# Kernel tuning notes

Measured on AMD Instinct MI355X. Metric: run time of the kernel, lower is better.

Reference implementation:

```python
import jax, jax.numpy as jnp
import numpy as np

BLOCK = 64  # block_size from config
NEG_INF = -1e9


def setup_inputs() -> dict:
    key = jax.random.key(0)
    k1, k2, k3, k4 = jax.random.split(key, 4)
    B, H, S, D = 2, 8, 2048, 64
    nb = S // BLOCK  # 32 blocks per side
    query = jax.random.normal(k1, (B, H, S, D), dtype=jnp.float32)
    key_t = jax.random.normal(k2, (B, H, S, D), dtype=jnp.float32)
    value = jax.random.normal(k3, (B, H, S, D), dtype=jnp.float32)
    # binary block mask; force diagonal blocks on so every row has >=1 valid key
    mat = jax.random.randint(k4, (nb, nb), 0, 2).astype(jnp.int32)
    mat = mat.at[jnp.arange(nb), jnp.arange(nb)].set(1)
    mask = jnp.ones((B, S), dtype=jnp.float32)  # padding mask (1 = keep)
    return {"query": query, "key": key_t, "value": value, "mask": mask, "mat": mat}


def reference(query, key, value, mask, mat):
    # Upsample block mask [nb, nb] -> dense [S, S] (nearest, like nn.Upsample)
    block_dense = jnp.repeat(jnp.repeat(mat, BLOCK, axis=0), BLOCK, axis=1) > 0
    # Block-sparse QK^T: only positions inside nonzero blocks participate.
    scores = jnp.einsum('bhqd,bhkd->bhqk', query, key)
    # Additive padding-mask bias, as in the original: 1e6 * (1 - mask)
    scores = scores - 1e6 * (1.0 - mask)[:, None, None, :]
    # Positions outside the block pattern are excluded from the softmax.
    scores = jnp.where(block_dense[None, None, :, :], scores, NEG_INF)
    attn = jax.nn.softmax(scores, axis=-1)
    out = jnp.einsum('bhqk,bhkd->bhqd', attn, value)
    return out
```

## Files before the change

kernel.cpp:

```cpp
#include <hip/hip_runtime.h>


typedef __attribute__((ext_vector_type(8))) short short8;
typedef __attribute__((ext_vector_type(4))) short short4_;
typedef __attribute__((ext_vector_type(4))) float float4_;
typedef __attribute__((ext_vector_type(8))) _Float16 half8_;

#define B_   2
#define H_   8
#define S_   2048
#define D_   64
#define NB_  32
#define KP   72
#define KP2  66
#define LOG2E 1.4426950408889634f

__device__ __forceinline__ short f2bf(float f) {
    union { float f; unsigned int u; } x; x.f = f;
    unsigned int r = x.u + 0x7FFFu + ((x.u >> 16) & 1u);
    return (short)(r >> 16);
}
__device__ __forceinline__ short f2bf_t(float f) {
    union { float f; unsigned int u; } x; x.f = f;
    return (short)(x.u >> 16);
}
__device__ __forceinline__ float bf2f(short s) {
    union { unsigned int u; float f; } x; x.u = ((unsigned int)(unsigned short)s) << 16;
    return x.f;
}
__device__ __forceinline__ short f2h(float f) {
    _Float16 h = (_Float16)f;
    return __builtin_bit_cast(short, h);
}
__device__ __forceinline__ int swz(int row, int gran) {
    return (row << 6) + (((gran ^ row) & 7) << 3);
}
__device__ __forceinline__ void gload16(const short* g, short* l) {
    __builtin_amdgcn_global_load_lds(
        (const __attribute__((address_space(1))) void*)g,
        (__attribute__((address_space(3))) void*)l, 16, 0, 0);
}
__device__ __forceinline__ void wg_remap(int n, int& bh, int& idx) {
    const int xcd = n & 7;
    const int sub = n >> 3;
    bh  = (xcd << 1) + (sub & 1);
    idx = sub >> 1;
}

__global__ __launch_bounds__(256)
void preconvert_kernel(const float* __restrict__ K, const float* __restrict__ V,
                       short* __restrict__ Khf, short* __restrict__ Vtb) {
    __shared__ short vn[64 * KP2];
    const int tid = threadIdx.x;
    int bh, kt;
    wg_remap(blockIdx.x, bh, kt);
    const size_t src = ((size_t)bh * S_ + kt * 64) * D_;
    const size_t dst = ((size_t)(bh * NB_ + kt)) << 12;

#pragma unroll
    for (int it = 0; it < 4; ++it) {
        int i = tid + it * 256;
        int row = i >> 4, c4 = (i & 15) * 4;
        float4_ kv = *(const float4_*)(K + src + row * D_ + c4);
        short4_ kh;
#pragma unroll
        for (int e = 0; e < 4; ++e) kh[e] = f2h(kv[e] * LOG2E);
        *(short4_*)(Khf + dst + swz(row, c4 >> 3) + (c4 & 7)) = kh;
        float4_ vv = *(const float4_*)(V + src + row * D_ + c4);
        short4_ vb;
#pragma unroll
        for (int e = 0; e < 4; ++e) vb[e] = f2bf(vv[e]);
        *(short4_*)&vn[row * KP2 + c4] = vb;
    }
    __syncthreads();

#pragma unroll
    for (int it = 0; it < 2; ++it) {
        int i = tid + it * 256;
        int d = i >> 3, g = i & 7;
        short8 o;
#pragma unroll
        for (int e = 0; e < 8; ++e) o[e] = vn[(g * 8 + e) * KP2 + d];
        *(short8*)(Vtb + dst + swz(d, g)) = o;
    }
}

__global__ __launch_bounds__(512, 4)
void attn_fused(const float* __restrict__ Q,
                const float* __restrict__ Msk,
                const int* __restrict__ Mat,
                float* __restrict__ O,
                const short* __restrict__ Khf_g,
                const short* __restrict__ Vtb_g) {
    __shared__ __align__(16) short lds[40960];

    const int tid  = threadIdx.x;
    const int wave = tid >> 6;
    const int half = wave >> 2;
    const int w4   = wave & 3;
    const int lane = tid & 63;
    const int c    = lane & 15;
    const int quad = lane >> 4;

    int bh, qb;
    wg_remap(blockIdx.x, bh, qb);
    const int b  = bh / H_;
    const size_t base = (size_t)bh * S_ * D_;

    unsigned long long bmv = __ballot(Mat[qb * NB_ + (lane & 31)] != 0);
    unsigned int mb = (unsigned int)(bmv & 0xFFFFFFFFull);
    const int nact  = __popc(mb);
    const int niter = (nact + 1) >> 1;
    unsigned int mine = 0;
    {
        unsigned int tb2 = mb; int idx = 0;
        while (tb2) {
            int k = __builtin_ctz(tb2); tb2 &= tb2 - 1;
            if ((idx & 1) == half) mine |= (1u << k);
            ++idx;
        }
    }

    int kb; bool kill;
    if (mine) { kb = __builtin_ctz(mine); mine &= mine - 1; kill = false; }
    else      { kb = __builtin_ctz(mb); kill = true; }
    {
        const size_t tb = ((size_t)(bh * NB_ + kb)) << 12;
        const int kd = (half << 12) + (w4 << 10);
        const short* gk = Khf_g + tb + (w4 << 10) + lane * 8;
        const short* gv = Vtb_g + tb + (w4 << 10) + lane * 8;
        gload16(gk,       &lds[kd]);
        gload16(gk + 512, &lds[kd + 512]);
        gload16(gv,       &lds[16384 + kd]);
        gload16(gv + 512, &lds[16384 + kd + 512]);
    }

    float biasc[4], biasn[4] = {0.f, 0.f, 0.f, 0.f};
#pragma unroll
    for (int t = 0; t < 4; ++t)
        biasc[t] = kill ? -2.0e6f
                        : -1.0e6f * LOG2E * (1.0f - Msk[(size_t)b * S_ + kb * 64 + t * 16 + c]);

    half8_ qa0, qa1;
    {
        const float* qp = Q + base + (size_t)(qb * 64 + w4 * 16 + c) * D_ + quad * 8;
        float4_ q0 = *(const float4_*)(qp);
        float4_ q1 = *(const float4_*)(qp + 4);
        float4_ q2 = *(const float4_*)(qp + 32);
        float4_ q3 = *(const float4_*)(qp + 36);
#pragma unroll
        for (int e = 0; e < 4; ++e) {
            qa0[e]     = (_Float16)q0[e];
            qa0[e + 4] = (_Float16)q1[e];
            qa1[e]     = (_Float16)q2[e];
            qa1[e + 4] = (_Float16)q3[e];
        }
    }

    float4_ o[4];
    float l_part[4];
#pragma unroll
    for (int t = 0; t < 4; ++t) { o[t][0] = 0.f; o[t][1] = 0.f; o[t][2] = 0.f; o[t][3] = 0.f; }
#pragma unroll
    for (int j = 0; j < 4; ++j) l_part[j] = 0.f;

    int foff_lo[4], foff_hi[4];
#pragma unroll
    for (int t = 0; t < 4; ++t) {
        foff_lo[t] = swz(t * 16 + c, quad);
        foff_hi[t] = swz(t * 16 + c, quad + 4);
    }
    const int pwoff = 32768 + (wave << 10);
    const int prd0  = pwoff + swz(c, quad);
    const int prd1  = pwoff + swz(c, quad + 4);

    int cur = 0;
    for (int it2 = 0; it2 < niter; ++it2) {
        bool nkill = true;
        if (it2 + 1 < niter && mine) { kb = __builtin_ctz(mine); mine &= mine - 1; nkill = false; }

        __syncthreads();

        if (it2 + 1 < niter) {
            const size_t tb = ((size_t)(bh * NB_ + kb)) << 12;
            const int kd = ((cur ^ 1) << 13) + (half << 12) + (w4 << 10);
            const short* gk = Khf_g + tb + (w4 << 10) + lane * 8;
            const short* gv = Vtb_g + tb + (w4 << 10) + lane * 8;
            gload16(gk,       &lds[kd]);
            gload16(gk + 512, &lds[kd + 512]);
            gload16(gv,       &lds[16384 + kd]);
            gload16(gv + 512, &lds[16384 + kd + 512]);
#pragma unroll
            for (int t = 0; t < 4; ++t)
                biasn[t] = nkill ? -2.0e6f
                                 : -1.0e6f * LOG2E * (1.0f - Msk[(size_t)b * S_ + kb * 64 + t * 16 + c]);
        }

        const int kbase = (cur << 13) + (half << 12);
        const int vbase = 16384 + kbase;

        float4_ sc[4];
#pragma unroll
        for (int t = 0; t < 4; ++t) { sc[t][0] = 0.f; sc[t][1] = 0.f; sc[t][2] = 0.f; sc[t][3] = 0.f; }
        __builtin_amdgcn_s_setprio(1);
#pragma unroll
        for (int t = 0; t < 4; ++t) {
            half8_ kf0 = __builtin_bit_cast(half8_, *(const short8*)&lds[kbase + foff_lo[t]]);
            half8_ kf1 = __builtin_bit_cast(half8_, *(const short8*)&lds[kbase + foff_hi[t]]);
            sc[t] = __builtin_amdgcn_mfma_f32_16x16x32_f16(qa0, kf0, sc[t], 0, 0, 0);
            sc[t] = __builtin_amdgcn_mfma_f32_16x16x32_f16(qa1, kf1, sc[t], 0, 0, 0);
        }
        __builtin_amdgcn_s_setprio(0);

#pragma unroll
        for (int t = 0; t < 4; ++t) {
            const int cg = (t << 1) + (c >> 3);
#pragma unroll
            for (int j = 0; j < 4; ++j) {
                float p = __builtin_amdgcn_exp2f(sc[t][j] + biasc[t]);
                l_part[j] += p;
                const int row = quad * 4 + j;
                lds[pwoff + (row << 6) + (((cg ^ row) & 7) << 3) + (c & 7)] = f2bf_t(p);
            }
        }

        short8 pa0 = *(const short8*)&lds[prd0];
        short8 pa1 = *(const short8*)&lds[prd1];

        __builtin_amdgcn_s_setprio(1);
#pragma unroll
        for (int t = 0; t < 4; ++t) {
            short8 vb0 = *(const short8*)&lds[vbase + foff_lo[t]];
            short8 vb1 = *(const short8*)&lds[vbase + foff_hi[t]];
            o[t] = __builtin_amdgcn_mfma_f32_16x16x32_bf16(pa0, vb0, o[t], 0, 0, 0);
            o[t] = __builtin_amdgcn_mfma_f32_16x16x32_bf16(pa1, vb1, o[t], 0, 0, 0);
        }
        __builtin_amdgcn_s_setprio(0);

#pragma unroll
        for (int t = 0; t < 4; ++t) biasc[t] = biasn[t];
        cur ^= 1;
    }

    __syncthreads();
    float* fl = (float*)lds;
    if (half == 1) {
        const int idx = ((wave - 4) * 64 + lane) * 21;
#pragma unroll
        for (int t = 0; t < 4; ++t)
#pragma unroll
            for (int j = 0; j < 4; ++j) fl[idx + t * 4 + j] = o[t][j];
#pragma unroll
        for (int j = 0; j < 4; ++j) fl[idx + 16 + j] = l_part[j];
    }
    __syncthreads();
    if (half == 0) {
        const int idx = (wave * 64 + lane) * 21;
#pragma unroll
        for (int j = 0; j < 4; ++j) {
            float rs = l_part[j] + fl[idx + 16 + j];
            rs += __shfl_xor(rs, 1);
            rs += __shfl_xor(rs, 2);
            rs += __shfl_xor(rs, 4);
            rs += __shfl_xor(rs, 8);
            float inv = 1.0f / rs;
            size_t rowoff = base + (size_t)(qb * 64 + w4 * 16 + quad * 4 + j) * D_;
#pragma unroll
            for (int t = 0; t < 4; ++t)
                O[rowoff + t * 16 + c] = (o[t][j] + fl[idx + t * 4 + j]) * inv;
        }
    }
}

__global__ __launch_bounds__(256, 2)
void attn_mfma_fb(const float* __restrict__ Q,
                  const float* __restrict__ K,
                  const float* __restrict__ V,
                  const float* __restrict__ Msk,
                  const int* __restrict__ Mat,
                  float* __restrict__ O) {
    __shared__ __align__(16) short lds[4 * 64 * KP];
    short* Khi = lds;
    short* Klo = lds + 64 * KP;
    short* Vt  = lds + 2 * 64 * KP;
    short* Pl  = lds + 3 * 64 * KP;

    const int tid  = threadIdx.x;
    const int wave = tid >> 6;
    const int lane = tid & 63;
    const int c    = lane & 15;
    const int quad = lane >> 4;

    const int qb = blockIdx.x;
    const int bh = blockIdx.y;
    const int b  = bh / H_;
    const size_t base = (size_t)bh * S_ * D_;

    short8 qh0, qh1, ql0, ql1;
    {
        const float* qp = Q + base + (size_t)(qb * 64 + wave * 16 + c) * D_ + quad * 8;
#pragma unroll
        for (int e = 0; e < 8; ++e) {
            float f0 = qp[e], f1 = qp[e + 32];
            qh0[e] = f2bf(f0); ql0[e] = f2bf(f0 - bf2f(qh0[e]));
            qh1[e] = f2bf(f1); ql1[e] = f2bf(f1 - bf2f(qh1[e]));
        }
    }

    float4_ o[4];
    float l_part[4];
#pragma unroll
    for (int t = 0; t < 4; ++t) { o[t][0] = 0.f; o[t][1] = 0.f; o[t][2] = 0.f; o[t][3] = 0.f; }
#pragma unroll
    for (int j = 0; j < 4; ++j) l_part[j] = 0.f;

    for (int kb = 0; kb < NB_; ++kb) {
        if (Mat[qb * NB_ + kb] == 0) continue;

        __syncthreads();
        {
            const float* kg = K + base + (size_t)kb * 64 * D_;
            const float* vg = V + base + (size_t)kb * 64 * D_;
#pragma unroll
            for (int it = 0; it < 4; ++it) {
                int i = tid + it * 256;
                int row = i >> 4, c4 = (i & 15) * 4;
                float4_ kv = *(const float4_*)(kg + row * D_ + c4);
                short4_ hi, lo;
#pragma unroll
                for (int e = 0; e < 4; ++e) {
                    hi[e] = f2bf(kv[e]);
                    lo[e] = f2bf(kv[e] - bf2f(hi[e]));
                }
                *(short4_*)&Khi[row * KP + c4] = hi;
                *(short4_*)&Klo[row * KP + c4] = lo;
                float4_ vv = *(const float4_*)(vg + row * D_ + c4);
#pragma unroll
                for (int e = 0; e < 4; ++e) Vt[(c4 + e) * KP + row] = f2bf(vv[e]);
            }
        }
        __syncthreads();

        float4_ sc[4];
#pragma unroll
        for (int t = 0; t < 4; ++t) { sc[t][0] = 0.f; sc[t][1] = 0.f; sc[t][2] = 0.f; sc[t][3] = 0.f; }
#pragma unroll
        for (int t = 0; t < 4; ++t) {
            const short* kph = &Khi[(t * 16 + c) * KP + quad * 8];
            const short* kpl = &Klo[(t * 16 + c) * KP + quad * 8];
            short8 kh0 = *(const short8*)(kph);
            short8 kh1 = *(const short8*)(kph + 32);
            short8 kl0 = *(const short8*)(kpl);
            short8 kl1 = *(const short8*)(kpl + 32);
            sc[t] = __builtin_amdgcn_mfma_f32_16x16x32_bf16(qh0, kh0, sc[t], 0, 0, 0);
            sc[t] = __builtin_amdgcn_mfma_f32_16x16x32_bf16(qh1, kh1, sc[t], 0, 0, 0);
            sc[t] = __builtin_amdgcn_mfma_f32_16x16x32_bf16(qh0, kl0, sc[t], 0, 0, 0);
            sc[t] = __builtin_amdgcn_mfma_f32_16x16x32_bf16(qh1, kl1, sc[t], 0, 0, 0);
            sc[t] = __builtin_amdgcn_mfma_f32_16x16x32_bf16(ql0, kh0, sc[t], 0, 0, 0);
            sc[t] = __builtin_amdgcn_mfma_f32_16x16x32_bf16(ql1, kh1, sc[t], 0, 0, 0);
        }

        short* Pw = Pl + wave * 16 * KP;
#pragma unroll
        for (int t = 0; t < 4; ++t) {
            float bias = -1.0e6f * (1.0f - Msk[(size_t)b * S_ + kb * 64 + t * 16 + c]);
#pragma unroll
            for (int j = 0; j < 4; ++j) {
                float p = __expf(sc[t][j] + bias);
                l_part[j] += p;
                Pw[(quad * 4 + j) * KP + t * 16 + c] = f2bf(p);
            }
        }

        const short* pp = Pl + wave * 16 * KP + c * KP + quad * 8;
        short8 pa0 = *(const short8*)(pp);
        short8 pa1 = *(const short8*)(pp + 32);

#pragma unroll
        for (int t = 0; t < 4; ++t) {
            const short* vp = &Vt[(t * 16 + c) * KP + quad * 8];
            short8 vb0 = *(const short8*)(vp);
            short8 vb1 = *(const short8*)(vp + 32);
            o[t] = __builtin_amdgcn_mfma_f32_16x16x32_bf16(pa0, vb0, o[t], 0, 0, 0);
            o[t] = __builtin_amdgcn_mfma_f32_16x16x32_bf16(pa1, vb1, o[t], 0, 0, 0);
        }
    }

#pragma unroll
    for (int j = 0; j < 4; ++j) {
        float rs = l_part[j];
        rs += __shfl_xor(rs, 1);
        rs += __shfl_xor(rs, 2);
        rs += __shfl_xor(rs, 4);
        rs += __shfl_xor(rs, 8);
        float inv = 1.0f / rs;
        size_t rowoff = base + (size_t)(qb * 64 + wave * 16 + quad * 4 + j) * D_;
#pragma unroll
        for (int t = 0; t < 4; ++t)
            O[rowoff + t * 16 + c] = o[t][j] * inv;
    }
}

extern "C" void kernel_launch(void* const* d_in, const int* in_sizes, int n_in,
                              void* d_out, int out_size, void* d_ws, size_t ws_size,
                              hipStream_t stream) {
    const float* q   = (const float*)d_in[0];
    const float* k   = (const float*)d_in[1];
    const float* v   = (const float*)d_in[2];
    const float* msk = (const float*)d_in[3];
    const int*   mat = (const int*)d_in[4];
    float*       out = (float*)d_out;

    const size_t elems = (size_t)B_ * H_ * S_ * D_;
    const size_t need  = 2 * elems * sizeof(short);
    const int use_pre  = (ws_size >= need) ? 1 : 0;

    short* khf = (short*)d_ws;
    short* vtb = khf + elems;

    if (use_pre) {
        preconvert_kernel<<<dim3(NB_ * B_ * H_), dim3(256), 0, stream>>>(k, v, khf, vtb);
        attn_fused<<<dim3(NB_ * B_ * H_), dim3(512), 0, stream>>>(q, msk, mat, out, khf, vtb);
    } else {
        dim3 grid(NB_, B_ * H_);
        attn_mfma_fb<<<grid, dim3(256), 0, stream>>>(q, k, v, msk, mat, out);
    }
}
```

Baseline: 104.7 us.

## Halve waves per block, each wave computes two 16-row query tiles

The fused attention kernel now launches 256 threads (4 waves) instead of 512. Each wave handles 32 query rows as two 16-row groups, so every K and V fragment read from LDS feeds two MFMAs. Each wave issues twice as many global-to-LDS loads, and the P scratch and the final cross-half reduction buffers are resized to match. The aim is fewer LDS reads and less sync overhead per unit of work, at the cost of higher register pressure, fewer waves to hide latency, and changed launch bounds.

```diff
diff --git a/kernel.cpp b/kernel.cpp
--- a/kernel.cpp
+++ b/kernel.cpp
@@ -85,7 +85,7 @@
     }
 }
 
-__global__ __launch_bounds__(512, 4)
+__global__ __launch_bounds__(256, 2)
 void attn_fused(const float* __restrict__ Q,
                 const float* __restrict__ Msk,
                 const int* __restrict__ Mat,
@@ -96,8 +96,8 @@
 
     const int tid  = threadIdx.x;
     const int wave = tid >> 6;
-    const int half = wave >> 2;
-    const int w4   = wave & 3;
+    const int half = wave >> 1;
+    const int wh   = wave & 1;
     const int lane = tid & 63;
     const int c    = lane & 15;
     const int quad = lane >> 4;
@@ -126,13 +126,14 @@
     else      { kb = __builtin_ctz(mb); kill = true; }
     {
         const size_t tb = ((size_t)(bh * NB_ + kb)) << 12;
-        const int kd = (half << 12) + (w4 << 10);
-        const short* gk = Khf_g + tb + (w4 << 10) + lane * 8;
-        const short* gv = Vtb_g + tb + (w4 << 10) + lane * 8;
-        gload16(gk,       &lds[kd]);
-        gload16(gk + 512, &lds[kd + 512]);
-        gload16(gv,       &lds[16384 + kd]);
-        gload16(gv + 512, &lds[16384 + kd + 512]);
+        const int kd = (half << 12) + (wh << 11);
+        const short* gk = Khf_g + tb + (wh << 11) + lane * 8;
+        const short* gv = Vtb_g + tb + (wh << 11) + lane * 8;
+#pragma unroll
+        for (int r = 0; r < 4; ++r) {
+            gload16(gk + r * 512, &lds[kd + r * 512]);
+            gload16(gv + r * 512, &lds[16384 + kd + r * 512]);
+        }
     }
 
     float biasc[4], biasn[4] = {0.f, 0.f, 0.f, 0.f};
@@ -141,28 +142,32 @@
         biasc[t] = kill ? -2.0e6f
                         : -1.0e6f * LOG2E * (1.0f - Msk[(size_t)b * S_ + kb * 64 + t * 16 + c]);
 
-    half8_ qa0, qa1;
-    {
-        const float* qp = Q + base + (size_t)(qb * 64 + w4 * 16 + c) * D_ + quad * 8;
+    half8_ qa[2][2];
+#pragma unroll
+    for (int g = 0; g < 2; ++g) {
+        const float* qp = Q + base + (size_t)(qb * 64 + wh * 32 + g * 16 + c) * D_ + quad * 8;
         float4_ q0 = *(const float4_*)(qp);
         float4_ q1 = *(const float4_*)(qp + 4);
         float4_ q2 = *(const float4_*)(qp + 32);
         float4_ q3 = *(const float4_*)(qp + 36);
 #pragma unroll
         for (int e = 0; e < 4; ++e) {
-            qa0[e]     = (_Float16)q0[e];
-            qa0[e + 4] = (_Float16)q1[e];
-            qa1[e]     = (_Float16)q2[e];
-            qa1[e + 4] = (_Float16)q3[e];
-        }
-    }
-
-    float4_ o[4];
-    float l_part[4];
-#pragma unroll
-    for (int t = 0; t < 4; ++t) { o[t][0] = 0.f; o[t][1] = 0.f; o[t][2] = 0.f; o[t][3] = 0.f; }
-#pragma unroll
-    for (int j = 0; j < 4; ++j) l_part[j] = 0.f;
+            qa[g][0][e]     = (_Float16)q0[e];
+            qa[g][0][e + 4] = (_Float16)q1[e];
+            qa[g][1][e]     = (_Float16)q2[e];
+            qa[g][1][e + 4] = (_Float16)q3[e];
+        }
+    }
+
+    float4_ o[2][4];
+    float l_part[2][4];
+#pragma unroll
+    for (int g = 0; g < 2; ++g)
+#pragma unroll
+        for (int t = 0; t < 4; ++t) {
+            o[g][t][0] = 0.f; o[g][t][1] = 0.f; o[g][t][2] = 0.f; o[g][t][3] = 0.f;
+            l_part[g][t] = 0.f;
+        }
 
     int foff_lo[4], foff_hi[4];
 #pragma unroll
@@ -170,7 +175,7 @@
         foff_lo[t] = swz(t * 16 + c, quad);
         foff_hi[t] = swz(t * 16 + c, quad + 4);
     }
-    const int pwoff = 32768 + (wave << 10);
+    const int pwoff = 32768 + (wave << 11);
     const int prd0  = pwoff + swz(c, quad);
     const int prd1  = pwoff + swz(c, quad + 4);
 
@@ -183,13 +188,14 @@
 
         if (it2 + 1 < niter) {
             const size_t tb = ((size_t)(bh * NB_ + kb)) << 12;
-            const int kd = ((cur ^ 1) << 13) + (half << 12) + (w4 << 10);
-            const short* gk = Khf_g + tb + (w4 << 10) + lane * 8;
-            const short* gv = Vtb_g + tb + (w4 << 10) + lane * 8;
-            gload16(gk,       &lds[kd]);
-            gload16(gk + 512, &lds[kd + 512]);
-            gload16(gv,       &lds[16384 + kd]);
-            gload16(gv + 512, &lds[16384 + kd + 512]);
+            const int kd = ((cur ^ 1) << 13) + (half << 12) + (wh << 11);
+            const short* gk = Khf_g + tb + (wh << 11) + lane * 8;
+            const short* gv = Vtb_g + tb + (wh << 11) + lane * 8;
+#pragma unroll
+            for (int r = 0; r < 4; ++r) {
+                gload16(gk + r * 512, &lds[kd + r * 512]);
+                gload16(gv + r * 512, &lds[16384 + kd + r * 512]);
+            }
 #pragma unroll
             for (int t = 0; t < 4; ++t)
                 biasn[t] = nkill ? -2.0e6f
@@ -199,41 +205,55 @@
         const int kbase = (cur << 13) + (half << 12);
         const int vbase = 16384 + kbase;
 
-        float4_ sc[4];
-#pragma unroll
-        for (int t = 0; t < 4; ++t) { sc[t][0] = 0.f; sc[t][1] = 0.f; sc[t][2] = 0.f; sc[t][3] = 0.f; }
+        float4_ sc[2][4];
+#pragma unroll
+        for (int g = 0; g < 2; ++g)
+#pragma unroll
+            for (int t = 0; t < 4; ++t) { sc[g][t][0] = 0.f; sc[g][t][1] = 0.f; sc[g][t][2] = 0.f; sc[g][t][3] = 0.f; }
         __builtin_amdgcn_s_setprio(1);
 #pragma unroll
         for (int t = 0; t < 4; ++t) {
             half8_ kf0 = __builtin_bit_cast(half8_, *(const short8*)&lds[kbase + foff_lo[t]]);
             half8_ kf1 = __builtin_bit_cast(half8_, *(const short8*)&lds[kbase + foff_hi[t]]);
-            sc[t] = __builtin_amdgcn_mfma_f32_16x16x32_f16(qa0, kf0, sc[t], 0, 0, 0);
-            sc[t] = __builtin_amdgcn_mfma_f32_16x16x32_f16(qa1, kf1, sc[t], 0, 0, 0);
+            sc[0][t] = __builtin_amdgcn_mfma_f32_16x16x32_f16(qa[0][0], kf0, sc[0][t], 0, 0, 0);
+            sc[0][t] = __builtin_amdgcn_mfma_f32_16x16x32_f16(qa[0][1], kf1, sc[0][t], 0, 0, 0);
+            sc[1][t] = __builtin_amdgcn_mfma_f32_16x16x32_f16(qa[1][0], kf0, sc[1][t], 0, 0, 0);
+            sc[1][t] = __builtin_amdgcn_mfma_f32_16x16x32_f16(qa[1][1], kf1, sc[1][t], 0, 0, 0);
         }
         __builtin_amdgcn_s_setprio(0);
 
 #pragma unroll
-        for (int t = 0; t < 4; ++t) {
-            const int cg = (t << 1) + (c >> 3);
-#pragma unroll
-            for (int j = 0; j < 4; ++j) {
-                float p = __builtin_amdgcn_exp2f(sc[t][j] + biasc[t]);
-                l_part[j] += p;
-                const int row = quad * 4 + j;
-                lds[pwoff + (row << 6) + (((cg ^ row) & 7) << 3) + (c & 7)] = f2bf_t(p);
+        for (int g = 0; g < 2; ++g) {
+            const int pg = pwoff + (g << 10);
+#pragma unroll
+            for (int t = 0; t < 4; ++t) {
+                const int cg = (t << 1) + (c >> 3);
+#pragma unroll
+                for (int j = 0; j < 4; ++j) {
+                    float p = __builtin_amdgcn_exp2f(sc[g][t][j] + biasc[t]);
+                    l_part[g][j] += p;
+                    const int row = quad * 4 + j;
+                    lds[pg + (row << 6) + (((cg ^ row) & 7) << 3) + (c & 7)] = f2bf_t(p);
+                }
             }
         }
 
-        short8 pa0 = *(const short8*)&lds[prd0];
-        short8 pa1 = *(const short8*)&lds[prd1];
+        short8 pa[2][2];
+#pragma unroll
+        for (int g = 0; g < 2; ++g) {
+            pa[g][0] = *(const short8*)&lds[prd0 + (g << 10)];
+            pa[g][1] = *(const short8*)&lds[prd1 + (g << 10)];
+        }
 
         __builtin_amdgcn_s_setprio(1);
 #pragma unroll
         for (int t = 0; t < 4; ++t) {
             short8 vb0 = *(const short8*)&lds[vbase + foff_lo[t]];
             short8 vb1 = *(const short8*)&lds[vbase + foff_hi[t]];
-            o[t] = __builtin_amdgcn_mfma_f32_16x16x32_bf16(pa0, vb0, o[t], 0, 0, 0);
-            o[t] = __builtin_amdgcn_mfma_f32_16x16x32_bf16(pa1, vb1, o[t], 0, 0, 0);
+            o[0][t] = __builtin_amdgcn_mfma_f32_16x16x32_bf16(pa[0][0], vb0, o[0][t], 0, 0, 0);
+            o[0][t] = __builtin_amdgcn_mfma_f32_16x16x32_bf16(pa[0][1], vb1, o[0][t], 0, 0, 0);
+            o[1][t] = __builtin_amdgcn_mfma_f32_16x16x32_bf16(pa[1][0], vb0, o[1][t], 0, 0, 0);
+            o[1][t] = __builtin_amdgcn_mfma_f32_16x16x32_bf16(pa[1][1], vb1, o[1][t], 0, 0, 0);
         }
         __builtin_amdgcn_s_setprio(0);
 
@@ -245,30 +265,35 @@
     __syncthreads();
     float* fl = (float*)lds;
     if (half == 1) {
-        const int idx = ((wave - 4) * 64 + lane) * 21;
-#pragma unroll
-        for (int t = 0; t < 4; ++t)
-#pragma unroll
-            for (int j = 0; j < 4; ++j) fl[idx + t * 4 + j] = o[t][j];
-#pragma unroll
-        for (int j = 0; j < 4; ++j) fl[idx + 16 + j] = l_part[j];
+        const int idx = ((wave - 2) * 64 + lane) * 41;
+#pragma unroll
+        for (int g = 0; g < 2; ++g) {
+#pragma unroll
+            for (int t = 0; t < 4; ++t)
+#pragma unroll
+                for (int j = 0; j < 4; ++j) fl[idx + g * 16 + t * 4 + j] = o[g][t][j];
+#pragma unroll
+            for (int j = 0; j < 4; ++j) fl[idx + 32 + g * 4 + j] = l_part[g][j];
+        }
     }
     __syncthreads();
     if (half == 0) {
-        const int idx = (wave * 64 + lane) * 21;
-#pragma unroll
-        for (int j = 0; j < 4; ++j) {
-            float rs = l_part[j] + fl[idx + 16 + j];
-            rs += __shfl_xor(rs, 1);
-            rs += __shfl_xor(rs, 2);
-            rs += __shfl_xor(rs, 4);
-            rs += __shfl_xor(rs, 8);
-            float inv = 1.0f / rs;
-            size_t rowoff = base + (size_t)(qb * 64 + w4 * 16 + quad * 4 + j) * D_;
-#pragma unroll
-            for (int t = 0; t < 4; ++t)
-                O[rowoff + t * 16 + c] = (o[t][j] + fl[idx + t * 4 + j]) * inv;
-        }
+        const int idx = (wave * 64 + lane) * 41;
+#pragma unroll
+        for (int g = 0; g < 2; ++g)
+#pragma unroll
+            for (int j = 0; j < 4; ++j) {
+                float rs = l_part[g][j] + fl[idx + 32 + g * 4 + j];
+                rs += __shfl_xor(rs, 1);
+                rs += __shfl_xor(rs, 2);
+                rs += __shfl_xor(rs, 4);
+                rs += __shfl_xor(rs, 8);
+                float inv = 1.0f / rs;
+                size_t rowoff = base + (size_t)(qb * 64 + wh * 32 + g * 16 + quad * 4 + j) * D_;
+#pragma unroll
+                for (int t = 0; t < 4; ++t)
+                    O[rowoff + t * 16 + c] = (o[g][t][j] + fl[idx + g * 16 + t * 4 + j]) * inv;
+            }
     }
 }
 
@@ -420,7 +445,7 @@
 
     if (use_pre) {
         preconvert_kernel<<<dim3(NB_ * B_ * H_), dim3(256), 0, stream>>>(k, v, khf, vtb);
-        attn_fused<<<dim3(NB_ * B_ * H_), dim3(512), 0, stream>>>(q, msk, mat, out, khf, vtb);
+        attn_fused<<<dim3(NB_ * B_ * H_), dim3(256), 0, stream>>>(q, msk, mat, out, khf, vtb);
     } else {
         dim3 grid(NB_, B_ * H_);
         attn_mfma_fb<<<grid, dim3(256), 0, stream>>>(q, k, v, msk, mat, out);
```

Result: no change. 105.3 us (+0.6%).

## Fuse K/V conversion into attention kernel, dropping the preconvert pass

Applied to the files above, without the earlier changes.

Removes the separate preconvert kernel and its fp16/bf16 workspace round trip. The attention kernel now loads fp32 K and V directly, converts them in registers and writes them into swizzled LDS, with the loads for the next block overlapped with the current block's MFMA work. The LOG2E scale moves from K onto Q. In exchange it gives up the async global_load_lds path, does scalar transposed LDS stores for V, reads K/V at double width from every query block, and raises register pressure. The unused fallback kernel is deleted.

```diff
diff --git a/kernel.cpp b/kernel.cpp
--- a/kernel.cpp
+++ b/kernel.cpp
@@ -11,8 +11,6 @@
 #define S_   2048
 #define D_   64
 #define NB_  32
-#define KP   72
-#define KP2  66
 #define LOG2E 1.4426950408889634f
 
 __device__ __forceinline__ short f2bf(float f) {
@@ -24,21 +22,12 @@
     union { float f; unsigned int u; } x; x.f = f;
     return (short)(x.u >> 16);
 }
-__device__ __forceinline__ float bf2f(short s) {
-    union { unsigned int u; float f; } x; x.u = ((unsigned int)(unsigned short)s) << 16;
-    return x.f;
-}
 __device__ __forceinline__ short f2h(float f) {
     _Float16 h = (_Float16)f;
     return __builtin_bit_cast(short, h);
 }
 __device__ __forceinline__ int swz(int row, int gran) {
     return (row << 6) + (((gran ^ row) & 7) << 3);
-}
-__device__ __forceinline__ void gload16(const short* g, short* l) {
-    __builtin_amdgcn_global_load_lds(
-        (const __attribute__((address_space(1))) void*)g,
-        (__attribute__((address_space(3))) void*)l, 16, 0, 0);
 }
 __device__ __forceinline__ void wg_remap(int n, int& bh, int& idx) {
     const int xcd = n & 7;
@@ -47,51 +36,13 @@
     idx = sub >> 1;
 }
 
-__global__ __launch_bounds__(256)
-void preconvert_kernel(const float* __restrict__ K, const float* __restrict__ V,
-                       short* __restrict__ Khf, short* __restrict__ Vtb) {
-    __shared__ short vn[64 * KP2];
-    const int tid = threadIdx.x;
-    int bh, kt;
-    wg_remap(blockIdx.x, bh, kt);
-    const size_t src = ((size_t)bh * S_ + kt * 64) * D_;
-    const size_t dst = ((size_t)(bh * NB_ + kt)) << 12;
-
-#pragma unroll
-    for (int it = 0; it < 4; ++it) {
-        int i = tid + it * 256;
-        int row = i >> 4, c4 = (i & 15) * 4;
-        float4_ kv = *(const float4_*)(K + src + row * D_ + c4);
-        short4_ kh;
-#pragma unroll
-        for (int e = 0; e < 4; ++e) kh[e] = f2h(kv[e] * LOG2E);
-        *(short4_*)(Khf + dst + swz(row, c4 >> 3) + (c4 & 7)) = kh;
-        float4_ vv = *(const float4_*)(V + src + row * D_ + c4);
-        short4_ vb;
-#pragma unroll
-        for (int e = 0; e < 4; ++e) vb[e] = f2bf(vv[e]);
-        *(short4_*)&vn[row * KP2 + c4] = vb;
-    }
-    __syncthreads();
-
-#pragma unroll
-    for (int it = 0; it < 2; ++it) {
-        int i = tid + it * 256;
-        int d = i >> 3, g = i & 7;
-        short8 o;
-#pragma unroll
-        for (int e = 0; e < 8; ++e) o[e] = vn[(g * 8 + e) * KP2 + d];
-        *(short8*)(Vtb + dst + swz(d, g)) = o;
-    }
-}
-
 __global__ __launch_bounds__(512, 4)
-void attn_fused(const float* __restrict__ Q,
-                const float* __restrict__ Msk,
-                const int* __restrict__ Mat,
-                float* __restrict__ O,
-                const short* __restrict__ Khf_g,
-                const short* __restrict__ Vtb_g) {
+void attn_direct(const float* __restrict__ Q,
+                 const float* __restrict__ K,
+                 const float* __restrict__ V,
+                 const float* __restrict__ Msk,
+                 const int* __restrict__ Mat,
+                 float* __restrict__ O) {
     __shared__ __align__(16) short lds[40960];
 
     const int tid  = threadIdx.x;
@@ -101,6 +52,13 @@
     const int lane = tid & 63;
     const int c    = lane & 15;
     const int quad = lane >> 4;
+    const int hid  = tid & 255;
+
+    const int krow   = hid >> 2;
+    const int kchunk = hid & 3;
+    const int kd0    = kchunk << 4;
+    const int vkey   = krow;
+    const int vd0    = kd0;
 
     int bh, qb;
     wg_remap(blockIdx.x, bh, qb);
@@ -125,14 +83,32 @@
     if (mine) { kb = __builtin_ctz(mine); mine &= mine - 1; kill = false; }
     else      { kb = __builtin_ctz(mb); kill = true; }
     {
-        const size_t tb = ((size_t)(bh * NB_ + kb)) << 12;
-        const int kd = (half << 12) + (w4 << 10);
-        const short* gk = Khf_g + tb + (w4 << 10) + lane * 8;
-        const short* gv = Vtb_g + tb + (w4 << 10) + lane * 8;
-        gload16(gk,       &lds[kd]);
-        gload16(gk + 512, &lds[kd + 512]);
-        gload16(gv,       &lds[16384 + kd]);
-        gload16(gv + 512, &lds[16384 + kd + 512]);
+        const float* kg = K + base + (size_t)kb * 64 * D_ + krow * D_ + kd0;
+        const float* vg = V + base + (size_t)kb * 64 * D_ + vkey * D_ + vd0;
+        const int kb0 = (half << 12);
+        const int vb0 = 16384 + (half << 12);
+        float4_ kv0 = *(const float4_*)(kg);
+        float4_ kv1 = *(const float4_*)(kg + 4);
+        float4_ kv2 = *(const float4_*)(kg + 8);
+        float4_ kv3 = *(const float4_*)(kg + 12);
+        short8 kw0, kw1;
+#pragma unroll
+        for (int e = 0; e < 4; ++e) {
+            kw0[e] = f2h(kv0[e]); kw0[e + 4] = f2h(kv1[e]);
+            kw1[e] = f2h(kv2[e]); kw1[e + 4] = f2h(kv3[e]);
+        }
+        *(short8*)&lds[kb0 + swz(krow, kchunk * 2)]     = kw0;
+        *(short8*)&lds[kb0 + swz(krow, kchunk * 2 + 1)] = kw1;
+        float4_ vv[4];
+#pragma unroll
+        for (int r = 0; r < 4; ++r) vv[r] = *(const float4_*)(vg + r * 4);
+#pragma unroll
+        for (int r = 0; r < 4; ++r)
+#pragma unroll
+            for (int e = 0; e < 4; ++e) {
+                int d = vd0 + r * 4 + e;
+                lds[vb0 + swz(d, vkey >> 3) + (vkey & 7)] = f2bf(vv[r][e]);
+            }
     }
 
     float biasc[4], biasn[4] = {0.f, 0.f, 0.f, 0.f};
@@ -150,10 +126,10 @@
         float4_ q3 = *(const float4_*)(qp + 36);
 #pragma unroll
         for (int e = 0; e < 4; ++e) {
-            qa0[e]     = (_Float16)q0[e];
-            qa0[e + 4] = (_Float16)q1[e];
-            qa1[e]     = (_Float16)q2[e];
-            qa1[e + 4] = (_Float16)q3[e];
+            qa0[e]     = (_Float16)(q0[e] * LOG2E);
+            qa0[e + 4] = (_Float16)(q1[e] * LOG2E);
+            qa1[e]     = (_Float16)(q2[e] * LOG2E);
+            qa1[e + 4] = (_Float16)(q3[e] * LOG2E);
         }
     }
 
@@ -178,18 +154,21 @@
     for (int it2 = 0; it2 < niter; ++it2) {
         bool nkill = true;
         if (it2 + 1 < niter && mine) { kb = __builtin_ctz(mine); mine &= mine - 1; nkill = false; }
+        const bool stage = (it2 + 1 < niter) && !nkill;
 
         __syncthreads();
 
+        const float* kg = nullptr; const float* vg = nullptr;
+        float4_ kv0, kv1, kv2, kv3;
+        if (stage) {
+            kg = K + base + (size_t)kb * 64 * D_ + krow * D_ + kd0;
+            vg = V + base + (size_t)kb * 64 * D_ + vkey * D_ + vd0;
+            kv0 = *(const float4_*)(kg);
+            kv1 = *(const float4_*)(kg + 4);
+            kv2 = *(const float4_*)(kg + 8);
+            kv3 = *(const float4_*)(kg + 12);
+        }
         if (it2 + 1 < niter) {
-            const size_t tb = ((size_t)(bh * NB_ + kb)) << 12;
-            const int kd = ((cur ^ 1) << 13) + (half << 12) + (w4 << 10);
-            const short* gk = Khf_g + tb + (w4 << 10) + lane * 8;
-            const short* gv = Vtb_g + tb + (w4 << 10) + lane * 8;
-            gload16(gk,       &lds[kd]);
-            gload16(gk + 512, &lds[kd + 512]);
-            gload16(gv,       &lds[16384 + kd]);
-            gload16(gv + 512, &lds[16384 + kd + 512]);
 #pragma unroll
             for (int t = 0; t < 4; ++t)
                 biasn[t] = nkill ? -2.0e6f
@@ -198,6 +177,7 @@
 
         const int kbase = (cur << 13) + (half << 12);
         const int vbase = 16384 + kbase;
+        const int nb13  = ((cur ^ 1) << 13) + (half << 12);
 
         float4_ sc[4];
 #pragma unroll
@@ -224,6 +204,20 @@
             }
         }
 
+        float4_ vv[4];
+        if (stage) {
+            short8 kw0, kw1;
+#pragma unroll
+            for (int e = 0; e < 4; ++e) {
+                kw0[e] = f2h(kv0[e]); kw0[e + 4] = f2h(kv1[e]);
+                kw1[e] = f2h(kv2[e]); kw1[e + 4] = f2h(kv3[e]);
+            }
+            *(short8*)&lds[nb13 + swz(krow, kchunk * 2)]     = kw0;
+            *(short8*)&lds[nb13 + swz(krow, kchunk * 2 + 1)] = kw1;
+#pragma unroll
+            for (int r = 0; r < 4; ++r) vv[r] = *(const float4_*)(vg + r * 4);
+        }
+
         short8 pa0 = *(const short8*)&lds[prd0];
         short8 pa1 = *(const short8*)&lds[prd1];
 
@@ -236,6 +230,17 @@
             o[t] = __builtin_amdgcn_mfma_f32_16x16x32_bf16(pa1, vb1, o[t], 0, 0, 0);
         }
         __builtin_amdgcn_s_setprio(0);
+
+        if (stage) {
+            const int vnb = 16384 + nb13;
+#pragma unroll
+            for (int r = 0; r < 4; ++r)
+#pragma unroll
+                for (int e = 0; e < 4; ++e) {
+                    int d = vd0 + r * 4 + e;
+                    lds[vnb + swz(d, vkey >> 3) + (vkey & 7)] = f2bf(vv[r][e]);
+                }
+        }
 
 #pragma unroll
         for (int t = 0; t < 4; ++t) biasc[t] = biasn[t];
@@ -269,135 +274,6 @@
             for (int t = 0; t < 4; ++t)
                 O[rowoff + t * 16 + c] = (o[t][j] + fl[idx + t * 4 + j]) * inv;
         }
-    }
-}
-
-__global__ __launch_bounds__(256, 2)
-void attn_mfma_fb(const float* __restrict__ Q,
-                  const float* __restrict__ K,
-                  const float* __restrict__ V,
-                  const float* __restrict__ Msk,
-                  const int* __restrict__ Mat,
-                  float* __restrict__ O) {
-    __shared__ __align__(16) short lds[4 * 64 * KP];
-    short* Khi = lds;
-    short* Klo = lds + 64 * KP;
-    short* Vt  = lds + 2 * 64 * KP;
-    short* Pl  = lds + 3 * 64 * KP;
-
-    const int tid  = threadIdx.x;
-    const int wave = tid >> 6;
-    const int lane = tid & 63;
-    const int c    = lane & 15;
-    const int quad = lane >> 4;
-
-    const int qb = blockIdx.x;
-    const int bh = blockIdx.y;
-    const int b  = bh / H_;
-    const size_t base = (size_t)bh * S_ * D_;
-
-    short8 qh0, qh1, ql0, ql1;
-    {
-        const float* qp = Q + base + (size_t)(qb * 64 + wave * 16 + c) * D_ + quad * 8;
-#pragma unroll
-        for (int e = 0; e < 8; ++e) {
-            float f0 = qp[e], f1 = qp[e + 32];
-            qh0[e] = f2bf(f0); ql0[e] = f2bf(f0 - bf2f(qh0[e]));
-            qh1[e] = f2bf(f1); ql1[e] = f2bf(f1 - bf2f(qh1[e]));
-        }
-    }
-
-    float4_ o[4];
-    float l_part[4];
-#pragma unroll
-    for (int t = 0; t < 4; ++t) { o[t][0] = 0.f; o[t][1] = 0.f; o[t][2] = 0.f; o[t][3] = 0.f; }
-#pragma unroll
-    for (int j = 0; j < 4; ++j) l_part[j] = 0.f;
-
-    for (int kb = 0; kb < NB_; ++kb) {
-        if (Mat[qb * NB_ + kb] == 0) continue;
-
-        __syncthreads();
-        {
-            const float* kg = K + base + (size_t)kb * 64 * D_;
-            const float* vg = V + base + (size_t)kb * 64 * D_;
-#pragma unroll
-            for (int it = 0; it < 4; ++it) {
-                int i = tid + it * 256;
-                int row = i >> 4, c4 = (i & 15) * 4;
-                float4_ kv = *(const float4_*)(kg + row * D_ + c4);
-                short4_ hi, lo;
-#pragma unroll
-                for (int e = 0; e < 4; ++e) {
-                    hi[e] = f2bf(kv[e]);
-                    lo[e] = f2bf(kv[e] - bf2f(hi[e]));
-                }
-                *(short4_*)&Khi[row * KP + c4] = hi;
-                *(short4_*)&Klo[row * KP + c4] = lo;
-                float4_ vv = *(const float4_*)(vg + row * D_ + c4);
-#pragma unroll
-                for (int e = 0; e < 4; ++e) Vt[(c4 + e) * KP + row] = f2bf(vv[e]);
-            }
-        }
-        __syncthreads();
-
-        float4_ sc[4];
-#pragma unroll
-        for (int t = 0; t < 4; ++t) { sc[t][0] = 0.f; sc[t][1] = 0.f; sc[t][2] = 0.f; sc[t][3] = 0.f; }
-#pragma unroll
-        for (int t = 0; t < 4; ++t) {
-            const short* kph = &Khi[(t * 16 + c) * KP + quad * 8];
-            const short* kpl = &Klo[(t * 16 + c) * KP + quad * 8];
-            short8 kh0 = *(const short8*)(kph);
-            short8 kh1 = *(const short8*)(kph + 32);
-            short8 kl0 = *(const short8*)(kpl);
-            short8 kl1 = *(const short8*)(kpl + 32);
-            sc[t] = __builtin_amdgcn_mfma_f32_16x16x32_bf16(qh0, kh0, sc[t], 0, 0, 0);
-            sc[t] = __builtin_amdgcn_mfma_f32_16x16x32_bf16(qh1, kh1, sc[t], 0, 0, 0);
-            sc[t] = __builtin_amdgcn_mfma_f32_16x16x32_bf16(qh0, kl0, sc[t], 0, 0, 0);
-            sc[t] = __builtin_amdgcn_mfma_f32_16x16x32_bf16(qh1, kl1, sc[t], 0, 0, 0);
-            sc[t] = __builtin_amdgcn_mfma_f32_16x16x32_bf16(ql0, kh0, sc[t], 0, 0, 0);
-            sc[t] = __builtin_amdgcn_mfma_f32_16x16x32_bf16(ql1, kh1, sc[t], 0, 0, 0);
-        }
-
-        short* Pw = Pl + wave * 16 * KP;
-#pragma unroll
-        for (int t = 0; t < 4; ++t) {
-            float bias = -1.0e6f * (1.0f - Msk[(size_t)b * S_ + kb * 64 + t * 16 + c]);
-#pragma unroll
-            for (int j = 0; j < 4; ++j) {
-                float p = __expf(sc[t][j] + bias);
-                l_part[j] += p;
-                Pw[(quad * 4 + j) * KP + t * 16 + c] = f2bf(p);
-            }
-        }
-
-        const short* pp = Pl + wave * 16 * KP + c * KP + quad * 8;
-        short8 pa0 = *(const short8*)(pp);
-        short8 pa1 = *(const short8*)(pp + 32);
-
-#pragma unroll
-        for (int t = 0; t < 4; ++t) {
-            const short* vp = &Vt[(t * 16 + c) * KP + quad * 8];
-            short8 vb0 = *(const short8*)(vp);
-            short8 vb1 = *(const short8*)(vp + 32);
-            o[t] = __builtin_amdgcn_mfma_f32_16x16x32_bf16(pa0, vb0, o[t], 0, 0, 0);
-            o[t] = __builtin_amdgcn_mfma_f32_16x16x32_bf16(pa1, vb1, o[t], 0, 0, 0);
-        }
-    }
-
-#pragma unroll
-    for (int j = 0; j < 4; ++j) {
-        float rs = l_part[j];
-        rs += __shfl_xor(rs, 1);
-        rs += __shfl_xor(rs, 2);
-        rs += __shfl_xor(rs, 4);
-        rs += __shfl_xor(rs, 8);
-        float inv = 1.0f / rs;
-        size_t rowoff = base + (size_t)(qb * 64 + wave * 16 + quad * 4 + j) * D_;
-#pragma unroll
-        for (int t = 0; t < 4; ++t)
-            O[rowoff + t * 16 + c] = o[t][j] * inv;
     }
 }
 
@@ -411,18 +287,7 @@
     const int*   mat = (const int*)d_in[4];
     float*       out = (float*)d_out;
 
-    const size_t elems = (size_t)B_ * H_ * S_ * D_;
-    const size_t need  = 2 * elems * sizeof(short);
-    const int use_pre  = (ws_size >= need) ? 1 : 0;
-
-    short* khf = (short*)d_ws;
-    short* vtb = khf + elems;
-
-    if (use_pre) {
-        preconvert_kernel<<<dim3(NB_ * B_ * H_), dim3(256), 0, stream>>>(k, v, khf, vtb);
-        attn_fused<<<dim3(NB_ * B_ * H_), dim3(512), 0, stream>>>(q, msk, mat, out, khf, vtb);
-    } else {
-        dim3 grid(NB_, B_ * H_);
-        attn_mfma_fb<<<grid, dim3(256), 0, stream>>>(q, k, v, msk, mat, out);
-    }
-}
+    (void)d_ws; (void)ws_size;
+
+    attn_direct<<<dim3(NB_ * B_ * H_), dim3(512), 0, stream>>>(q, k, v, msk, mat, out);
+}
```

New measurement: 165.4 us. 1.58x slower.

## Keep P in registers via transposed QK MFMA and permlane swaps instead of LDS

Applied to the files above, without the earlier changes.

Swaps the MFMA operand order so the score tile comes out transposed (keys along rows), then converts P to packed bf16 with v_cvt_pk_bf16 and rearranges it into the PV A-operand layout using v_permlane16/32_swap. This removes the per-wave LDS round trip for P, shrinking shared memory, and simplifies the row-sum reduction. It also skips loading the next tile when that tile is killed, and loads the padding-mask values as vectors inside the loop instead of prefetching the bias. P rounding changes from truncation to the hardware packed conversion, and the permlane shuffling must map lanes exactly to the PV operand layout.

```diff
diff --git a/kernel.cpp b/kernel.cpp
--- a/kernel.cpp
+++ b/kernel.cpp
@@ -4,6 +4,7 @@
 typedef __attribute__((ext_vector_type(8))) short short8;
 typedef __attribute__((ext_vector_type(4))) short short4_;
 typedef __attribute__((ext_vector_type(4))) float float4_;
+typedef __attribute__((ext_vector_type(4))) unsigned int uint4_;
 typedef __attribute__((ext_vector_type(8))) _Float16 half8_;
 
 #define B_   2
@@ -20,10 +21,6 @@
     unsigned int r = x.u + 0x7FFFu + ((x.u >> 16) & 1u);
     return (short)(r >> 16);
 }
-__device__ __forceinline__ short f2bf_t(float f) {
-    union { float f; unsigned int u; } x; x.f = f;
-    return (short)(x.u >> 16);
-}
 __device__ __forceinline__ float bf2f(short s) {
     union { unsigned int u; float f; } x; x.u = ((unsigned int)(unsigned short)s) << 16;
     return x.f;
@@ -39,6 +36,11 @@
     __builtin_amdgcn_global_load_lds(
         (const __attribute__((address_space(1))) void*)g,
         (__attribute__((address_space(3))) void*)l, 16, 0, 0);
+}
+__device__ __forceinline__ unsigned int cvt_pk_bf16(float lo, float hi) {
+    unsigned int r;
+    asm("v_cvt_pk_bf16_f32 %0, %1, %2" : "=v"(r) : "v"(lo), "v"(hi));
+    return r;
 }
 __device__ __forceinline__ void wg_remap(int n, int& bh, int& idx) {
     const int xcd = n & 7;
@@ -73,7 +75,6 @@
         *(short4_*)&vn[row * KP2 + c4] = vb;
     }
     __syncthreads();
-
 #pragma unroll
     for (int it = 0; it < 2; ++it) {
         int i = tid + it * 256;
@@ -92,7 +93,7 @@
                 float* __restrict__ O,
                 const short* __restrict__ Khf_g,
                 const short* __restrict__ Vtb_g) {
-    __shared__ __align__(16) short lds[40960];
+    __shared__ __align__(16) short lds[32768];
 
     const int tid  = threadIdx.x;
     const int wave = tid >> 6;
@@ -101,6 +102,7 @@
     const int lane = tid & 63;
     const int c    = lane & 15;
     const int quad = lane >> 4;
+    const bool oddq = (quad & 1) != 0;
 
     int bh, qb;
     wg_remap(blockIdx.x, bh, qb);
@@ -121,11 +123,11 @@
         }
     }
 
-    int kb; bool kill;
-    if (mine) { kb = __builtin_ctz(mine); mine &= mine - 1; kill = false; }
-    else      { kb = __builtin_ctz(mb); kill = true; }
+    int kb_c; bool kill_c;
+    if (mine) { kb_c = __builtin_ctz(mine); mine &= mine - 1; kill_c = false; }
+    else      { kb_c = __builtin_ctz(mb); kill_c = true; }
     {
-        const size_t tb = ((size_t)(bh * NB_ + kb)) << 12;
+        const size_t tb = ((size_t)(bh * NB_ + kb_c)) << 12;
         const int kd = (half << 12) + (w4 << 10);
         const short* gk = Khf_g + tb + (w4 << 10) + lane * 8;
         const short* gv = Vtb_g + tb + (w4 << 10) + lane * 8;
@@ -135,12 +137,6 @@
         gload16(gv + 512, &lds[16384 + kd + 512]);
     }
 
-    float biasc[4], biasn[4] = {0.f, 0.f, 0.f, 0.f};
-#pragma unroll
-    for (int t = 0; t < 4; ++t)
-        biasc[t] = kill ? -2.0e6f
-                        : -1.0e6f * LOG2E * (1.0f - Msk[(size_t)b * S_ + kb * 64 + t * 16 + c]);
-
     half8_ qa0, qa1;
     {
         const float* qp = Q + base + (size_t)(qb * 64 + w4 * 16 + c) * D_ + quad * 8;
@@ -158,11 +154,9 @@
     }
 
     float4_ o[4];
-    float l_part[4];
+    float l_sum = 0.f;
 #pragma unroll
     for (int t = 0; t < 4; ++t) { o[t][0] = 0.f; o[t][1] = 0.f; o[t][2] = 0.f; o[t][3] = 0.f; }
-#pragma unroll
-    for (int j = 0; j < 4; ++j) l_part[j] = 0.f;
 
     int foff_lo[4], foff_hi[4];
 #pragma unroll
@@ -170,19 +164,16 @@
         foff_lo[t] = swz(t * 16 + c, quad);
         foff_hi[t] = swz(t * 16 + c, quad + 4);
     }
-    const int pwoff = 32768 + (wave << 10);
-    const int prd0  = pwoff + swz(c, quad);
-    const int prd1  = pwoff + swz(c, quad + 4);
 
     int cur = 0;
     for (int it2 = 0; it2 < niter; ++it2) {
-        bool nkill = true;
-        if (it2 + 1 < niter && mine) { kb = __builtin_ctz(mine); mine &= mine - 1; nkill = false; }
+        int kb_n = kb_c; bool kill_n = true;
+        if (it2 + 1 < niter && mine) { kb_n = __builtin_ctz(mine); mine &= mine - 1; kill_n = false; }
 
         __syncthreads();
 
-        if (it2 + 1 < niter) {
-            const size_t tb = ((size_t)(bh * NB_ + kb)) << 12;
+        if (it2 + 1 < niter && !kill_n) {
+            const size_t tb = ((size_t)(bh * NB_ + kb_n)) << 12;
             const int kd = ((cur ^ 1) << 13) + (half << 12) + (w4 << 10);
             const short* gk = Khf_g + tb + (w4 << 10) + lane * 8;
             const short* gv = Vtb_g + tb + (w4 << 10) + lane * 8;
@@ -190,15 +181,18 @@
             gload16(gk + 512, &lds[kd + 512]);
             gload16(gv,       &lds[16384 + kd]);
             gload16(gv + 512, &lds[16384 + kd + 512]);
-#pragma unroll
-            for (int t = 0; t < 4; ++t)
-                biasn[t] = nkill ? -2.0e6f
-                                 : -1.0e6f * LOG2E * (1.0f - Msk[(size_t)b * S_ + kb * 64 + t * 16 + c]);
         }
 
         const int kbase = (cur << 13) + (half << 12);
         const int vbase = 16384 + kbase;
 
+        float4_ mskv[4];
+        if (!kill_c) {
+#pragma unroll
+            for (int t = 0; t < 4; ++t)
+                mskv[t] = *(const float4_*)(Msk + (size_t)b * S_ + kb_c * 64 + t * 16 + quad * 4);
+        }
+
         float4_ sc[4];
 #pragma unroll
         for (int t = 0; t < 4; ++t) { sc[t][0] = 0.f; sc[t][1] = 0.f; sc[t][2] = 0.f; sc[t][3] = 0.f; }
@@ -207,25 +201,54 @@
         for (int t = 0; t < 4; ++t) {
             half8_ kf0 = __builtin_bit_cast(half8_, *(const short8*)&lds[kbase + foff_lo[t]]);
             half8_ kf1 = __builtin_bit_cast(half8_, *(const short8*)&lds[kbase + foff_hi[t]]);
-            sc[t] = __builtin_amdgcn_mfma_f32_16x16x32_f16(qa0, kf0, sc[t], 0, 0, 0);
-            sc[t] = __builtin_amdgcn_mfma_f32_16x16x32_f16(qa1, kf1, sc[t], 0, 0, 0);
+            sc[t] = __builtin_amdgcn_mfma_f32_16x16x32_f16(kf0, qa0, sc[t], 0, 0, 0);
+            sc[t] = __builtin_amdgcn_mfma_f32_16x16x32_f16(kf1, qa1, sc[t], 0, 0, 0);
         }
         __builtin_amdgcn_s_setprio(0);
 
-#pragma unroll
-        for (int t = 0; t < 4; ++t) {
-            const int cg = (t << 1) + (c >> 3);
+        unsigned int r_[4][2];
+#pragma unroll
+        for (int t = 0; t < 4; ++t) {
+            float p[4];
 #pragma unroll
             for (int j = 0; j < 4; ++j) {
-                float p = __builtin_amdgcn_exp2f(sc[t][j] + biasc[t]);
-                l_part[j] += p;
-                const int row = quad * 4 + j;
-                lds[pwoff + (row << 6) + (((cg ^ row) & 7) << 3) + (c & 7)] = f2bf_t(p);
+                float bj = kill_c ? -2.0e6f : -1.0e6f * LOG2E * (1.0f - mskv[t][j]);
+                p[j] = __builtin_amdgcn_exp2f(sc[t][j] + bj);
+                l_sum += p[j];
             }
-        }
-
-        short8 pa0 = *(const short8*)&lds[prd0];
-        short8 pa1 = *(const short8*)&lds[prd1];
+            r_[t][0] = cvt_pk_bf16(p[0], p[1]);
+            r_[t][1] = cvt_pk_bf16(p[2], p[3]);
+        }
+
+        unsigned int La[4][2], Lb[4][2];
+#pragma unroll
+        for (int t = 0; t < 4; ++t)
+#pragma unroll
+            for (int s = 0; s < 2; ++s) {
+                unsigned int x = r_[t][s], y = r_[t][s];
+                asm("v_permlane16_swap_b32 %0, %1" : "+v"(x), "+v"(y));
+                La[t][s] = x;
+                Lb[t][s] = y;
+            }
+        uint4_ w0, w1;
+#pragma unroll
+        for (int s = 0; s < 2; ++s) {
+            unsigned int d0, s1;
+            d0 = La[0][s]; s1 = La[1][s];
+            asm("v_permlane32_swap_b32 %0, %1" : "+v"(d0), "+v"(s1));
+            w0[s] = oddq ? s1 : d0;
+            d0 = Lb[0][s]; s1 = Lb[1][s];
+            asm("v_permlane32_swap_b32 %0, %1" : "+v"(d0), "+v"(s1));
+            w0[2 + s] = oddq ? s1 : d0;
+            d0 = La[2][s]; s1 = La[3][s];
+            asm("v_permlane32_swap_b32 %0, %1" : "+v"(d0), "+v"(s1));
+            w1[s] = oddq ? s1 : d0;
+            d0 = Lb[2][s]; s1 = Lb[3][s];
+            asm("v_permlane32_swap_b32 %0, %1" : "+v"(d0), "+v"(s1));
+            w1[2 + s] = oddq ? s1 : d0;
+        }
+        short8 pa0 = __builtin_bit_cast(short8, w0);
+        short8 pa1 = __builtin_bit_cast(short8, w1);
 
         __builtin_amdgcn_s_setprio(1);
 #pragma unroll
@@ -237,32 +260,28 @@
         }
         __builtin_amdgcn_s_setprio(0);
 
-#pragma unroll
-        for (int t = 0; t < 4; ++t) biasc[t] = biasn[t];
-        cur ^= 1;
+        kb_c = kb_n; kill_c = kill_n; cur ^= 1;
     }
 
     __syncthreads();
     float* fl = (float*)lds;
     if (half == 1) {
-        const int idx = ((wave - 4) * 64 + lane) * 21;
+        const int idx = ((wave - 4) * 64 + lane) * 17;
 #pragma unroll
         for (int t = 0; t < 4; ++t)
 #pragma unroll
             for (int j = 0; j < 4; ++j) fl[idx + t * 4 + j] = o[t][j];
-#pragma unroll
-        for (int j = 0; j < 4; ++j) fl[idx + 16 + j] = l_part[j];
+        fl[idx + 16] = l_sum;
     }
     __syncthreads();
     if (half == 0) {
-        const int idx = (wave * 64 + lane) * 21;
+        const int idx = (wave * 64 + lane) * 17;
+        float lt = l_sum + fl[idx + 16];
+        lt += __shfl_xor(lt, 16);
+        lt += __shfl_xor(lt, 32);
 #pragma unroll
         for (int j = 0; j < 4; ++j) {
-            float rs = l_part[j] + fl[idx + 16 + j];
-            rs += __shfl_xor(rs, 1);
-            rs += __shfl_xor(rs, 2);
-            rs += __shfl_xor(rs, 4);
-            rs += __shfl_xor(rs, 8);
+            float rs = __shfl(lt, quad * 4 + j, 16);
             float inv = 1.0f / rs;
             size_t rowoff = base + (size_t)(qb * 64 + w4 * 16 + quad * 4 + j) * D_;
 #pragma unroll
```

After: 106.8 us. +2.0%, slower.
